# Kernel tuning notes

Measured on AMD Instinct MI355X. Metric: run time of the kernel, lower is better.

The kernel has to match this reference:

```python
import jax, jax.numpy as jnp
import numpy as np

N = 50000      # nodes
E = 800000     # edges (before self-loops)
IN = 128       # in_channels
HID = 64       # hidden_channels
HEADS = 2
OUT = 128      # out_channels
NEG_SLOPE = 0.2


def setup_inputs() -> dict:
    key = jax.random.key(0)
    ks = jax.random.split(key, 12)
    p = lambda k, shape: jax.random.normal(k, shape, dtype=jnp.float32) * 0.05
    return {
        "x": jax.random.normal(ks[0], (N, IN), dtype=jnp.float32),
        "edge_index": jax.random.randint(ks[1], (2, E), 0, N, dtype=jnp.int32),
        "W1": p(ks[2], (IN, HEADS * HID)),
        "a_src1": p(ks[3], (HEADS, HID)),
        "a_dst1": p(ks[4], (HEADS, HID)),
        "b1": jnp.zeros((HEADS * HID,), dtype=jnp.float32),
        "W2": p(ks[5], (HEADS * HID, OUT)),
        "a_src2": p(ks[6], (1, OUT)),
        "a_dst2": p(ks[7], (1, OUT)),
        "b2": jnp.zeros((OUT,), dtype=jnp.float32),
    }


def _gat_conv(x, src, dst, W, a_src, a_dst, b, heads, out_c, concat):
    n = x.shape[0]
    h = (x @ W).reshape(n, heads, out_c)                # [N,H,C]
    al_s = jnp.sum(h * a_src, axis=-1)                  # [N,H]
    al_d = jnp.sum(h * a_dst, axis=-1)                  # [N,H]
    e = jax.nn.leaky_relu(al_s[src] + al_d[dst], NEG_SLOPE)  # [E',H]
    # softmax over edges grouped by destination node (numerically stable)
    e_max = jax.ops.segment_max(e, dst, num_segments=n)
    ee = jnp.exp(e - e_max[dst])
    denom = jax.ops.segment_sum(ee, dst, num_segments=n)
    alpha = ee / (denom[dst] + 1e-16)                   # [E',H]
    out = jax.ops.segment_sum(alpha[:, :, None] * h[src], dst, num_segments=n)  # [N,H,C]
    out = out.reshape(n, heads * out_c) if concat else out.mean(axis=1)
    return out + b


def reference(x, edge_index, W1, a_src1, a_dst1, b1, W2, a_src2, a_dst2, b2):
    n = x.shape[0]
    loops = jnp.arange(n, dtype=edge_index.dtype)       # PyG GATConv adds self-loops
    src = jnp.concatenate([edge_index[0], loops])
    dst = jnp.concatenate([edge_index[1], loops])
    h = jax.nn.elu(_gat_conv(x, src, dst, W1, a_src1, a_dst1, b1, HEADS, HID, True))
    return _gat_conv(h, src, dst, W2, a_src2, a_dst2, b2, 1, OUT, False)
```

## Files before the change

### kernel.cpp

```cpp
#include <hip/hip_runtime.h>
#include <hip/hip_bf16.h>
#include <math.h>

#define N_NODES 50000
#define N_EDGES 800000
#define NEG_SLOPE 0.2f
#define NBUCK ((N_NODES + 255) / 256)
#define CCHUNK 4096
#define DCAP 8192

__device__ inline float lrelu(float x) { return fmaxf(x, NEG_SLOPE * x); }

__device__ inline unsigned bf16rne(float f) {
    unsigned u = __float_as_uint(f);
    return (u + 0x7fffu + ((u >> 16) & 1u)) >> 16;
}

__global__ __launch_bounds__(256) void bucketcount_kernel(const int* __restrict__ ei,
                                                          int* __restrict__ gbcnt) {
    __shared__ int lc[NBUCK];
    for (int i = threadIdx.x; i < NBUCK; i += 256) lc[i] = 0;
    __syncthreads();
    int stride = gridDim.x * 256;
    for (int e = blockIdx.x * 256 + threadIdx.x; e < N_EDGES; e += stride)
        atomicAdd(&lc[ei[N_EDGES + e] >> 8], 1);
    __syncthreads();
    for (int i = threadIdx.x; i < NBUCK; i += 256)
        if (lc[i]) atomicAdd(&gbcnt[i], lc[i]);
}

__global__ __launch_bounds__(256) void bucketscan_kernel(const int* __restrict__ gbcnt,
                                                         int* __restrict__ bbase,
                                                         int* __restrict__ bcur) {
    __shared__ int ss[256];
    int t = threadIdx.x;
    int v = (t < NBUCK) ? gbcnt[t] : 0;
    ss[t] = v;
    __syncthreads();
    for (int d = 1; d < 256; d <<= 1) {
        int u = (t >= d) ? ss[t - d] : 0;
        __syncthreads();
        ss[t] += u;
        __syncthreads();
    }
    int excl = ss[t] - v;
    if (t < NBUCK) { bbase[t] = excl; bcur[t] = excl; }
    if (t == 0) bbase[NBUCK] = N_EDGES;
}

__global__ __launch_bounds__(256) void bucketscatter_kernel(const int* __restrict__ ei,
                                                            int* __restrict__ bcur,
                                                            int2* __restrict__ bpairs) {
    __shared__ int cnt[NBUCK], startl[NBUCK], baseg[NBUCK], cur2[NBUCK];
    __shared__ int ss[256];
    __shared__ int2 stage[CCHUNK];
    int t = threadIdx.x;
    int e0 = blockIdx.x * CCHUNK;
    int nume = min(CCHUNK, N_EDGES - e0);
    for (int i = t; i < NBUCK; i += 256) { cnt[i] = 0; cur2[i] = 0; }
    __syncthreads();
    int src[CCHUNK / 256], dst[CCHUNK / 256];
    #pragma unroll
    for (int j = 0; j < CCHUNK / 256; ++j) {
        int idx = t + j * 256;
        if (idx < nume) {
            src[j] = ei[e0 + idx];
            dst[j] = ei[N_EDGES + e0 + idx];
            atomicAdd(&cnt[dst[j] >> 8], 1);
        } else dst[j] = -1;
    }
    __syncthreads();
    {
        int v = (t < NBUCK) ? cnt[t] : 0;
        ss[t] = v;
        __syncthreads();
        for (int d = 1; d < 256; d <<= 1) {
            int u = (t >= d) ? ss[t - d] : 0;
            __syncthreads();
            ss[t] += u;
            __syncthreads();
        }
        if (t < NBUCK) startl[t] = ss[t] - v;
    }
    __syncthreads();
    if (t < NBUCK && cnt[t] > 0) baseg[t] = atomicAdd(&bcur[t], cnt[t]);
    __syncthreads();
    #pragma unroll
    for (int j = 0; j < CCHUNK / 256; ++j) {
        if (dst[j] >= 0) {
            int b = dst[j] >> 8;
            int slot = startl[b] + atomicAdd(&cur2[b], 1);
            stage[slot] = make_int2(src[j], dst[j]);
        }
    }
    __syncthreads();
    for (int i = t; i < nume; i += 256) {
        int2 p = stage[i];
        int b = p.y >> 8;
        bpairs[baseg[b] + (i - startl[b])] = p;
    }
}

__global__ __launch_bounds__(256) void csrfinalize_kernel(const int2* __restrict__ bpairs,
                                                          const int* __restrict__ bbase,
                                                          int* __restrict__ ptr,
                                                          int* __restrict__ csr) {
    __shared__ int cnt[256], excl[256], cur[256];
    __shared__ int ss[256];
    __shared__ int2 P[DCAP];
    int b = blockIdx.x, t = threadIdx.x;
    int bb = bbase[b], be = bbase[b + 1];
    int n = be - bb;
    int d0 = b << 8;
    int dmax = min(256, N_NODES - d0);
    bool fits = (n <= DCAP);
    cnt[t] = 0; cur[t] = 0;
    __syncthreads();
    for (int i = t; i < n; i += 256) {
        int2 p = bpairs[bb + i];
        if (fits) P[i] = p;
        atomicAdd(&cnt[p.y & 255], 1);
    }
    __syncthreads();
    {
        int v = cnt[t];
        ss[t] = v;
        __syncthreads();
        for (int d = 1; d < 256; d <<= 1) {
            int u = (t >= d) ? ss[t - d] : 0;
            __syncthreads();
            ss[t] += u;
            __syncthreads();
        }
        excl[t] = ss[t] - v;
    }
    __syncthreads();
    if (t < dmax) ptr[d0 + t] = bb + excl[t];
    if (b == NBUCK - 1 && t == 0) ptr[N_NODES] = N_EDGES;
    for (int i = t; i < n; i += 256) {
        int2 p = fits ? P[i] : bpairs[bb + i];
        int ld = p.y & 255;
        int pos = bb + excl[ld] + atomicAdd(&cur[ld], 1);
        csr[pos] = p.x;
    }
}

#define GB_ROWS 64
template <int H>
__global__ __launch_bounds__(256) void gemm_kernel(const float* __restrict__ X,
                                                   const float* __restrict__ W,
                                                   const float* __restrict__ asrc,
                                                   const float* __restrict__ adst,
                                                   unsigned short* __restrict__ Hb,
                                                   float* __restrict__ als,
                                                   float* __restrict__ ald,
                                                   int nrows) {
    __shared__ float xt[GB_ROWS][132];
    const int tid = threadIdx.x;
    const int r0 = blockIdx.x * GB_ROWS;
    #pragma unroll
    for (int i = 0; i < 8; ++i) {
        int idx = tid + 256 * i;
        int r = idx >> 5, c4 = (idx & 31) * 4;
        int gr = r0 + r;
        float4 v = make_float4(0.f, 0.f, 0.f, 0.f);
        if (gr < nrows) v = *(const float4*)(X + (size_t)gr * 128 + c4);
        *(float4*)(&xt[r][c4]) = v;
    }
    __syncthreads();
    const int c0 = (tid & 31) * 4;
    const int rbase = (tid >> 5) * 8;
    const int q = tid & 31;
    float acc[8][4];
    #pragma unroll
    for (int i = 0; i < 8; ++i)
        #pragma unroll
        for (int j = 0; j < 4; ++j) acc[i][j] = 0.f;
    #pragma unroll 4
    for (int k = 0; k < 128; ++k) {
        float4 w4 = *(const float4*)(W + k * 128 + c0);
        float xv[8];
        #pragma unroll
        for (int i = 0; i < 8; ++i) xv[i] = xt[rbase + i][k];
        #pragma unroll
        for (int i = 0; i < 8; ++i) {
            acc[i][0] = fmaf(xv[i], w4.x, acc[i][0]);
            acc[i][1] = fmaf(xv[i], w4.y, acc[i][1]);
            acc[i][2] = fmaf(xv[i], w4.z, acc[i][2]);
            acc[i][3] = fmaf(xv[i], w4.w, acc[i][3]);
        }
    }
    float4 as4 = *(const float4*)(asrc + c0);
    float4 ad4 = *(const float4*)(adst + c0);
    #pragma unroll
    for (int i = 0; i < 8; ++i) {
        int gr = r0 + rbase + i;
        bool ok = gr < nrows;
        if (ok) {
            uint2 p;
            p.x = bf16rne(acc[i][0]) | (bf16rne(acc[i][1]) << 16);
            p.y = bf16rne(acc[i][2]) | (bf16rne(acc[i][3]) << 16);
            *(uint2*)(Hb + (size_t)gr * 128 + c0) = p;
        }
        float sp = acc[i][0] * as4.x + acc[i][1] * as4.y + acc[i][2] * as4.z + acc[i][3] * as4.w;
        float dp = acc[i][0] * ad4.x + acc[i][1] * ad4.y + acc[i][2] * ad4.z + acc[i][3] * ad4.w;
        #pragma unroll
        for (int off = 1; off < (H == 2 ? 16 : 32); off <<= 1) {
            sp += __shfl_xor(sp, off);
            dp += __shfl_xor(dp, off);
        }
        if (ok) {
            if (H == 2) {
                if (q == 0)  { als[(size_t)gr * 2]     = sp; ald[(size_t)gr * 2]     = dp; }
                if (q == 16) { als[(size_t)gr * 2 + 1] = sp; ald[(size_t)gr * 2 + 1] = dp; }
            } else {
                if (q == 0) { als[gr] = sp; ald[gr] = dp; }
            }
        }
    }
}

template <int H, int DO_ELU>
__global__ __launch_bounds__(256) void aggregate_kernel(const unsigned short* __restrict__ Hb,
                                                        const float* __restrict__ als,
                                                        const float* __restrict__ aldv,
                                                        const int* __restrict__ ptr,
                                                        const int* __restrict__ csr,
                                                        const float* __restrict__ bias,
                                                        float* __restrict__ out) {
    __shared__ int   s_src[4][64];
    __shared__ float s_p[4][H][64];
    const int w = threadIdx.x >> 6;
    const int lane = threadIdx.x & 63;
    const int d = blockIdx.x * 4 + w;
    if (d >= N_NODES) return;
    const int head = (H == 2) ? (lane >> 5) : 0;

    int beg = ptr[d], end = ptr[d + 1];

    float ald0, ald1 = 0.f, es0, es1 = 0.f;
    if (H == 2) {
        float2 ta = *(const float2*)(aldv + (size_t)d * 2);
        float2 ts = *(const float2*)(als + (size_t)d * 2);
        ald0 = ta.x; ald1 = ta.y;
        es0 = lrelu(ts.x + ald0); es1 = lrelu(ts.y + ald1);
    } else {
        ald0 = aldv[d]; es0 = lrelu(als[d] + ald0);
    }

    int k0 = beg + lane;
    int src0 = 0;
    float e0 = -INFINITY, e1 = -INFINITY;
    if (k0 < end) {
        src0 = csr[k0];
        if (H == 2) {
            float2 t = *(const float2*)(als + (size_t)src0 * 2);
            e0 = lrelu(t.x + ald0); e1 = lrelu(t.y + ald1);
        } else e0 = lrelu(als[src0] + ald0);
    }
    float m0 = fmaxf(es0, e0);
    float m1 = (H == 2) ? fmaxf(es1, e1) : 0.f;
    for (int k = k0 + 64; k < end; k += 64) {
        int s = csr[k];
        if (H == 2) {
            float2 t = *(const float2*)(als + (size_t)s * 2);
            m0 = fmaxf(m0, lrelu(t.x + ald0));
            m1 = fmaxf(m1, lrelu(t.y + ald1));
        } else m0 = fmaxf(m0, lrelu(als[s] + ald0));
    }
    #pragma unroll
    for (int off = 32; off; off >>= 1) {
        m0 = fmaxf(m0, __shfl_xor(m0, off));
        if (H == 2) m1 = fmaxf(m1, __shfl_xor(m1, off));
    }

    float l0 = 0.f, l1 = 0.f;
    float ax0 = 0.f, ay0 = 0.f, ax1 = 0.f, ay1 = 0.f;
    float ax2 = 0.f, ay2 = 0.f, ax3 = 0.f, ay3 = 0.f;

    for (int t0 = beg; t0 < end; t0 += 64) {
        int cnt = min(64, end - t0);
        int k = t0 + lane;
        if (k < end) {
            int s; float f0, f1 = 0.f;
            if (t0 == beg) { s = src0; f0 = e0; f1 = e1; }
            else {
                s = csr[k];
                if (H == 2) {
                    float2 t = *(const float2*)(als + (size_t)s * 2);
                    f0 = lrelu(t.x + ald0); f1 = lrelu(t.y + ald1);
                } else f0 = lrelu(als[s] + ald0);
            }
            float p0 = __expf(f0 - m0);
            l0 += p0;
            s_src[w][lane] = s;
            s_p[w][0][lane] = p0;
            if (H == 2) {
                float p1 = __expf(f1 - m1);
                l1 += p1;
                s_p[w][1][lane] = p1;
            }
        }
        int j = 0;
        for (; j + 3 < cnt; j += 4) {
            int sA = s_src[w][j],     sB = s_src[w][j + 1];
            int sC = s_src[w][j + 2], sD = s_src[w][j + 3];
            float pA = s_p[w][head][j],     pB = s_p[w][head][j + 1];
            float pC = s_p[w][head][j + 2], pD = s_p[w][head][j + 3];
            unsigned uA = ((const unsigned*)(Hb + (size_t)sA * 128))[lane];
            unsigned uB = ((const unsigned*)(Hb + (size_t)sB * 128))[lane];
            unsigned uC = ((const unsigned*)(Hb + (size_t)sC * 128))[lane];
            unsigned uD = ((const unsigned*)(Hb + (size_t)sD * 128))[lane];
            ax0 = fmaf(pA, __uint_as_float(uA << 16), ax0);
            ay0 = fmaf(pA, __uint_as_float(uA & 0xffff0000u), ay0);
            ax1 = fmaf(pB, __uint_as_float(uB << 16), ax1);
            ay1 = fmaf(pB, __uint_as_float(uB & 0xffff0000u), ay1);
            ax2 = fmaf(pC, __uint_as_float(uC << 16), ax2);
            ay2 = fmaf(pC, __uint_as_float(uC & 0xffff0000u), ay2);
            ax3 = fmaf(pD, __uint_as_float(uD << 16), ax3);
            ay3 = fmaf(pD, __uint_as_float(uD & 0xffff0000u), ay3);
        }
        for (; j < cnt; ++j) {
            int sA = s_src[w][j];
            float pA = s_p[w][head][j];
            unsigned uA = ((const unsigned*)(Hb + (size_t)sA * 128))[lane];
            ax0 = fmaf(pA, __uint_as_float(uA << 16), ax0);
            ay0 = fmaf(pA, __uint_as_float(uA & 0xffff0000u), ay0);
        }
    }

    float ax = (ax0 + ax1) + (ax2 + ax3);
    float ay = (ay0 + ay1) + (ay2 + ay3);
    float mh  = (head == 0) ? m0 : m1;
    float esh = (head == 0) ? es0 : es1;
    float psh = __expf(esh - mh);
    {
        unsigned u = ((const unsigned*)(Hb + (size_t)d * 128))[lane];
        ax = fmaf(psh, __uint_as_float(u << 16), ax);
        ay = fmaf(psh, __uint_as_float(u & 0xffff0000u), ay);
    }
    #pragma unroll
    for (int off = 32; off; off >>= 1) {
        l0 += __shfl_xor(l0, off);
        if (H == 2) l1 += __shfl_xor(l1, off);
    }
    float denom = ((head == 0) ? l0 : l1) + psh;
    float inv = 1.f / (denom + 1e-16f);
    float o0 = ax * inv + bias[2 * lane];
    float o1 = ay * inv + bias[2 * lane + 1];
    if (DO_ELU) {
        o0 = o0 > 0.f ? o0 : expm1f(o0);
        o1 = o1 > 0.f ? o1 : expm1f(o1);
    }
    ((float2*)(out + (size_t)d * 128))[lane] = make_float2(o0, o1);
}

extern "C" void kernel_launch(void* const* d_in, const int* in_sizes, int n_in,
                              void* d_out, int out_size, void* d_ws, size_t ws_size,
                              hipStream_t stream) {
    const float* x      = (const float*)d_in[0];
    const int*   ei     = (const int*)d_in[1];
    const float* W1     = (const float*)d_in[2];
    const float* a_src1 = (const float*)d_in[3];
    const float* a_dst1 = (const float*)d_in[4];
    const float* b1     = (const float*)d_in[5];
    const float* W2     = (const float*)d_in[6];
    const float* a_src2 = (const float*)d_in[7];
    const float* a_dst2 = (const float*)d_in[8];
    const float* b2     = (const float*)d_in[9];
    float* out = (float*)d_out;

    char* ws = (char*)d_ws;
    size_t off = 0;
    auto alloc = [&](size_t bytes) { void* p = ws + off; off += (bytes + 255) & ~(size_t)255; return p; };
    int*   ptr    = (int*)alloc((N_NODES + 1) * sizeof(int));
    int*   gbcnt  = (int*)alloc(NBUCK * sizeof(int));
    int*   bbase  = (int*)alloc((NBUCK + 1) * sizeof(int));
    int*   bcur   = (int*)alloc(NBUCK * sizeof(int));
    int2*  bpairs = (int2*)alloc((size_t)N_EDGES * sizeof(int2));
    int*   csr    = (int*)alloc(N_EDGES * sizeof(int));
    float* x2     = (float*)alloc((size_t)N_NODES * 128 * sizeof(float));
    unsigned short* hb = (unsigned short*)alloc((size_t)N_NODES * 128 * sizeof(unsigned short));
    float* als    = (float*)alloc(N_NODES * 2 * sizeof(float));
    float* ald    = (float*)alloc(N_NODES * 2 * sizeof(float));

    hipMemsetAsync(gbcnt, 0, NBUCK * sizeof(int), stream);
    bucketcount_kernel<<<256, 256, 0, stream>>>(ei, gbcnt);
    bucketscan_kernel<<<1, 256, 0, stream>>>(gbcnt, bbase, bcur);
    bucketscatter_kernel<<<(N_EDGES + CCHUNK - 1) / CCHUNK, 256, 0, stream>>>(ei, bcur, bpairs);
    csrfinalize_kernel<<<NBUCK, 256, 0, stream>>>(bpairs, bbase, ptr, csr);

    int gblocks = (N_NODES + GB_ROWS - 1) / GB_ROWS;
    int wblocks = (N_NODES + 3) / 4;

    gemm_kernel<2><<<gblocks, 256, 0, stream>>>(x, W1, a_src1, a_dst1, hb, als, ald, N_NODES);
    aggregate_kernel<2, 1><<<wblocks, 256, 0, stream>>>(hb, als, ald, ptr, csr, b1, x2);

    gemm_kernel<1><<<gblocks, 256, 0, stream>>>(x2, W2, a_src2, a_dst2, hb, als, ald, N_NODES);
    aggregate_kernel<1, 0><<<wblocks, 256, 0, stream>>>(hb, als, ald, ptr, csr, b2, out);
}
```

Before: 191.8 us.

## Halve GEMM row tile, unroll gather by 8, replace memset with kernel

The GEMM tile drops from 64 to 32 rows per block, giving each thread 4 accumulator rows instead of 8. This doubles the block count for better occupancy but reloads W more often. The aggregation gather loop now unrolls by 8 with eight accumulator pairs and 4/2/1 tails, so more independent row loads are in flight, at the cost of extra registers. The hipMemsetAsync on the bucket counters becomes a tiny zeroing kernel to cut launch overhead.

New measurement: 197.0 us. 2.7% more time.

```diff
diff --git a/kernel.cpp b/kernel.cpp
--- a/kernel.cpp
+++ b/kernel.cpp
@@ -14,6 +14,11 @@
 __device__ inline unsigned bf16rne(float f) {
     unsigned u = __float_as_uint(f);
     return (u + 0x7fffu + ((u >> 16) & 1u)) >> 16;
+}
+
+__global__ void zerobuf_kernel(int* __restrict__ p) {
+    int i = threadIdx.x;
+    if (i < NBUCK) p[i] = 0;
 }
 
 __global__ __launch_bounds__(256) void bucketcount_kernel(const int* __restrict__ ei,
@@ -145,7 +150,7 @@
     }
 }
 
-#define GB_ROWS 64
+#define GB_ROWS 32
 template <int H>
 __global__ __launch_bounds__(256) void gemm_kernel(const float* __restrict__ X,
                                                    const float* __restrict__ W,
@@ -159,7 +164,7 @@
     const int tid = threadIdx.x;
     const int r0 = blockIdx.x * GB_ROWS;
     #pragma unroll
-    for (int i = 0; i < 8; ++i) {
+    for (int i = 0; i < 4; ++i) {
         int idx = tid + 256 * i;
         int r = idx >> 5, c4 = (idx & 31) * 4;
         int gr = r0 + r;
@@ -169,21 +174,21 @@
     }
     __syncthreads();
     const int c0 = (tid & 31) * 4;
-    const int rbase = (tid >> 5) * 8;
+    const int rbase = (tid >> 5) * 4;
     const int q = tid & 31;
-    float acc[8][4];
-    #pragma unroll
-    for (int i = 0; i < 8; ++i)
+    float acc[4][4];
+    #pragma unroll
+    for (int i = 0; i < 4; ++i)
         #pragma unroll
         for (int j = 0; j < 4; ++j) acc[i][j] = 0.f;
     #pragma unroll 4
     for (int k = 0; k < 128; ++k) {
         float4 w4 = *(const float4*)(W + k * 128 + c0);
-        float xv[8];
+        float xv[4];
         #pragma unroll
-        for (int i = 0; i < 8; ++i) xv[i] = xt[rbase + i][k];
+        for (int i = 0; i < 4; ++i) xv[i] = xt[rbase + i][k];
         #pragma unroll
-        for (int i = 0; i < 8; ++i) {
+        for (int i = 0; i < 4; ++i) {
             acc[i][0] = fmaf(xv[i], w4.x, acc[i][0]);
             acc[i][1] = fmaf(xv[i], w4.y, acc[i][1]);
             acc[i][2] = fmaf(xv[i], w4.z, acc[i][2]);
@@ -193,7 +198,7 @@
     float4 as4 = *(const float4*)(asrc + c0);
     float4 ad4 = *(const float4*)(adst + c0);
     #pragma unroll
-    for (int i = 0; i < 8; ++i) {
+    for (int i = 0; i < 4; ++i) {
         int gr = r0 + rbase + i;
         bool ok = gr < nrows;
         if (ok) {
@@ -275,8 +280,9 @@
     }
 
     float l0 = 0.f, l1 = 0.f;
-    float ax0 = 0.f, ay0 = 0.f, ax1 = 0.f, ay1 = 0.f;
-    float ax2 = 0.f, ay2 = 0.f, ax3 = 0.f, ay3 = 0.f;
+    float ax[8], ay[8];
+    #pragma unroll
+    for (int i = 0; i < 8; ++i) { ax[i] = 0.f; ay[i] = 0.f; }
 
     for (int t0 = beg; t0 < end; t0 += 64) {
         int cnt = min(64, end - t0);
@@ -302,42 +308,62 @@
             }
         }
         int j = 0;
-        for (; j + 3 < cnt; j += 4) {
-            int sA = s_src[w][j],     sB = s_src[w][j + 1];
-            int sC = s_src[w][j + 2], sD = s_src[w][j + 3];
-            float pA = s_p[w][head][j],     pB = s_p[w][head][j + 1];
-            float pC = s_p[w][head][j + 2], pD = s_p[w][head][j + 3];
-            unsigned uA = ((const unsigned*)(Hb + (size_t)sA * 128))[lane];
-            unsigned uB = ((const unsigned*)(Hb + (size_t)sB * 128))[lane];
-            unsigned uC = ((const unsigned*)(Hb + (size_t)sC * 128))[lane];
-            unsigned uD = ((const unsigned*)(Hb + (size_t)sD * 128))[lane];
-            ax0 = fmaf(pA, __uint_as_float(uA << 16), ax0);
-            ay0 = fmaf(pA, __uint_as_float(uA & 0xffff0000u), ay0);
-            ax1 = fmaf(pB, __uint_as_float(uB << 16), ax1);
-            ay1 = fmaf(pB, __uint_as_float(uB & 0xffff0000u), ay1);
-            ax2 = fmaf(pC, __uint_as_float(uC << 16), ax2);
-            ay2 = fmaf(pC, __uint_as_float(uC & 0xffff0000u), ay2);
-            ax3 = fmaf(pD, __uint_as_float(uD << 16), ax3);
-            ay3 = fmaf(pD, __uint_as_float(uD & 0xffff0000u), ay3);
-        }
-        for (; j < cnt; ++j) {
+        for (; j + 7 < cnt; j += 8) {
+            int ss[8]; float pp[8]; unsigned uu[8];
+            #pragma unroll
+            for (int i = 0; i < 8; ++i) { ss[i] = s_src[w][j + i]; pp[i] = s_p[w][head][j + i]; }
+            #pragma unroll
+            for (int i = 0; i < 8; ++i) uu[i] = ((const unsigned*)(Hb + (size_t)ss[i] * 128))[lane];
+            #pragma unroll
+            for (int i = 0; i < 8; ++i) {
+                ax[i] = fmaf(pp[i], __uint_as_float(uu[i] << 16), ax[i]);
+                ay[i] = fmaf(pp[i], __uint_as_float(uu[i] & 0xffff0000u), ay[i]);
+            }
+        }
+        if (j + 3 < cnt) {
+            int ss[4]; float pp[4]; unsigned uu[4];
+            #pragma unroll
+            for (int i = 0; i < 4; ++i) { ss[i] = s_src[w][j + i]; pp[i] = s_p[w][head][j + i]; }
+            #pragma unroll
+            for (int i = 0; i < 4; ++i) uu[i] = ((const unsigned*)(Hb + (size_t)ss[i] * 128))[lane];
+            #pragma unroll
+            for (int i = 0; i < 4; ++i) {
+                ax[i] = fmaf(pp[i], __uint_as_float(uu[i] << 16), ax[i]);
+                ay[i] = fmaf(pp[i], __uint_as_float(uu[i] & 0xffff0000u), ay[i]);
+            }
+            j += 4;
+        }
+        if (j + 1 < cnt) {
+            int ss[2]; float pp[2]; unsigned uu[2];
+            #pragma unroll
+            for (int i = 0; i < 2; ++i) { ss[i] = s_src[w][j + i]; pp[i] = s_p[w][head][j + i]; }
+            #pragma unroll
+            for (int i = 0; i < 2; ++i) uu[i] = ((const unsigned*)(Hb + (size_t)ss[i] * 128))[lane];
+            #pragma unroll
+            for (int i = 0; i < 2; ++i) {
+                ax[i] = fmaf(pp[i], __uint_as_float(uu[i] << 16), ax[i]);
+                ay[i] = fmaf(pp[i], __uint_as_float(uu[i] & 0xffff0000u), ay[i]);
+            }
+            j += 2;
+        }
+        if (j < cnt) {
             int sA = s_src[w][j];
             float pA = s_p[w][head][j];
             unsigned uA = ((const unsigned*)(Hb + (size_t)sA * 128))[lane];
-            ax0 = fmaf(pA, __uint_as_float(uA << 16), ax0);
-            ay0 = fmaf(pA, __uint_as_float(uA & 0xffff0000u), ay0);
-        }
-    }
-
-    float ax = (ax0 + ax1) + (ax2 + ax3);
-    float ay = (ay0 + ay1) + (ay2 + ay3);
+            ax[0] = fmaf(pA, __uint_as_float(uA << 16), ax[0]);
+            ay[0] = fmaf(pA, __uint_as_float(uA & 0xffff0000u), ay[0]);
+        }
+    }
+
+    float axs = ((ax[0] + ax[1]) + (ax[2] + ax[3])) + ((ax[4] + ax[5]) + (ax[6] + ax[7]));
+    float ays = ((ay[0] + ay[1]) + (ay[2] + ay[3])) + ((ay[4] + ay[5]) + (ay[6] + ay[7]));
     float mh  = (head == 0) ? m0 : m1;
     float esh = (head == 0) ? es0 : es1;
     float psh = __expf(esh - mh);
     {
         unsigned u = ((const unsigned*)(Hb + (size_t)d * 128))[lane];
-        ax = fmaf(psh, __uint_as_float(u << 16), ax);
-        ay = fmaf(psh, __uint_as_float(u & 0xffff0000u), ay);
+        axs = fmaf(psh, __uint_as_float(u << 16), axs);
+        ays = fmaf(psh, __uint_as_float(u & 0xffff0000u), ays);
     }
     #pragma unroll
     for (int off = 32; off; off >>= 1) {
@@ -346,8 +372,8 @@
     }
     float denom = ((head == 0) ? l0 : l1) + psh;
     float inv = 1.f / (denom + 1e-16f);
-    float o0 = ax * inv + bias[2 * lane];
-    float o1 = ay * inv + bias[2 * lane + 1];
+    float o0 = axs * inv + bias[2 * lane];
+    float o1 = ays * inv + bias[2 * lane + 1];
     if (DO_ELU) {
         o0 = o0 > 0.f ? o0 : expm1f(o0);
         o1 = o1 > 0.f ? o1 : expm1f(o1);
@@ -384,7 +410,7 @@
     float* als    = (float*)alloc(N_NODES * 2 * sizeof(float));
     float* ald    = (float*)alloc(N_NODES * 2 * sizeof(float));
 
-    hipMemsetAsync(gbcnt, 0, NBUCK * sizeof(int), stream);
+    zerobuf_kernel<<<1, 256, 0, stream>>>(gbcnt);
     bucketcount_kernel<<<256, 256, 0, stream>>>(ei, gbcnt);
     bucketscan_kernel<<<1, 256, 0, stream>>>(gbcnt, bbase, bcur);
     bucketscatter_kernel<<<(N_EDGES + CCHUNK - 1) / CCHUNK, 256, 0, stream>>>(ei, bcur, bpairs);
```
